# Performance work log

Hardware: AMD Instinct MI355X
Metric: run time of the kernel (lower is better)

The kernel has to match this reference:

```python
import jax, jax.numpy as jnp
import numpy as np

SCORE_THRESHOLD = 0.5
IOU_THRESHOLD = 0.5


def _pairwise_iou(boxes):
    # boxes: [N, 4] in xyxy
    x1, y1, x2, y2 = boxes[:, 0], boxes[:, 1], boxes[:, 2], boxes[:, 3]
    area = (x2 - x1) * (y2 - y1)  # [N]
    ix1 = jnp.maximum(x1[:, None], x1[None, :])
    iy1 = jnp.maximum(y1[:, None], y1[None, :])
    ix2 = jnp.minimum(x2[:, None], x2[None, :])
    iy2 = jnp.minimum(y2[:, None], y2[None, :])
    iw = jnp.clip(ix2 - ix1, 0.0)
    ih = jnp.clip(iy2 - iy1, 0.0)
    inter = iw * ih  # [N, N]
    union = area[:, None] + area[None, :] - inter
    return inter / jnp.maximum(union, 1e-9)


def setup_inputs() -> dict:
    key = jax.random.key(0)
    rtdetr_raw_out = jax.random.uniform(key, (1, 8192, 5), dtype=jnp.float32)
    return {"rtdetr_raw_out": rtdetr_raw_out}


def reference(rtdetr_raw_out):
    x = rtdetr_raw_out[0]                      # [N, 5]
    cxcywh = x[:, :4]
    conf = x[:, 4]
    conf = conf / jnp.max(conf)                # normalize by max score
    cx, cy, w, h = cxcywh[:, 0], cxcywh[:, 1], cxcywh[:, 2], cxcywh[:, 3]
    xyxy = jnp.stack([cx - w * 0.5, cy - h * 0.5, cx + w * 0.5, cy + h * 0.5], axis=1)
    valid = conf >= SCORE_THRESHOLD            # score filter
    N = xyxy.shape[0]
    # sort by descending score (torchvision nms processes boxes in score order)
    order = jnp.argsort(-conf)
    boxes_s = xyxy[order]
    scores_s = conf[order]
    valid_s = valid[order]
    iou = _pairwise_iou(boxes_s)               # [N, N]
    idx = jnp.arange(N)

    def body(i, keep):
        # if box i survives, suppress all lower-score boxes with IoU > thr
        sup = keep[i] & (iou[i] > IOU_THRESHOLD) & (idx > i)
        return keep & ~sup

    keep = jax.lax.fori_loop(0, N, body, valid_s)
    out = jnp.concatenate([boxes_s, scores_s[:, None]], axis=1)  # [N, 5]
    # fixed-shape output: suppressed / below-threshold rows are zeroed
    return jnp.where(keep[:, None], out, 0.0)
```

## Files before the change

### kernel.cpp

```cpp
#include <hip/hip_runtime.h>
#include <cstdint>

typedef unsigned long long ull;

#define N_BOX 8192
#define N_WORDS 128
#define CH 512
#define WPC 8
#define NBLK 16

#define OFF_TB     0
#define OFF_TC     3440640
#define OFF_TD     3932160
#define OFF_BOXES  4456448
#define OFF_SCORES 4587520
#define OFF_RANK   4620288
#define OFF_MAXC   4653056
#define OFF_CTRL   4653120
#define OFF_KEPT   4653248

__device__ __forceinline__ int rows_before2(int c) {
    return 7424 * c - 256 * c * c;
}

__device__ __forceinline__ ull make_key(float s, int idx) {
    return (((ull)__float_as_uint(s)) << 13) | (ull)(8191 - idx);
}

__device__ __forceinline__ float box_area(float4 b) {
    return __fmul_rn(__fsub_rn(b.z, b.x), __fsub_rn(b.w, b.y));
}

__device__ __forceinline__ bool iou_gt_half(float4 a, float aarea, float4 b, float barea) {
    float ix1 = fmaxf(a.x, b.x);
    float iy1 = fmaxf(a.y, b.y);
    float ix2 = fminf(a.z, b.z);
    float iy2 = fminf(a.w, b.w);
    float iw = fmaxf(__fsub_rn(ix2, ix1), 0.0f);
    float ih = fmaxf(__fsub_rn(iy2, iy1), 0.0f);
    float inter = __fmul_rn(iw, ih);
    float uni = __fsub_rn(__fadd_rn(aarea, barea), inter);
    float iou = __fdiv_rn(inter, fmaxf(uni, 1e-9f));
    return iou > 0.5f;
}

__global__ __launch_bounds__(256) void k1_max_zero(const float* __restrict__ in,
                                                   int* __restrict__ maxci,
                                                   int* __restrict__ rank,
                                                   int* __restrict__ ctrl) {
    int t = threadIdx.x;
    int i = blockIdx.x * 256 + t;
    float c = in[i * 5 + 4];
    for (int off = 32; off; off >>= 1) c = fmaxf(c, __shfl_down(c, off));
    __shared__ float wm[4];
    if ((t & 63) == 0) wm[t >> 6] = c;
    __syncthreads();
    if (t == 0) {
        float m = fmaxf(fmaxf(wm[0], wm[1]), fmaxf(wm[2], wm[3]));
        atomicMax(maxci, __float_as_int(m));
    }
    if (blockIdx.x == 0 && t < 32) ctrl[t] = 0;
    rank[i] = 0;
}

__global__ __launch_bounds__(256) void k2_rank(const float* __restrict__ in,
                                               const float* __restrict__ maxc_p,
                                               int* __restrict__ rank) {
    __shared__ ull keys[1024];
    int t = threadIdx.x;
    int bx = blockIdx.x;
    int it = bx & 31;
    int jt = bx >> 5;
    float maxc = *maxc_p;
    for (int r = 0; r < 4; ++r) {
        int j = jt * 1024 + r * 256 + t;
        float s = __fdiv_rn(in[j * 5 + 4], maxc);
        keys[r * 256 + t] = make_key(s, j);
    }
    __syncthreads();
    int i = it * 256 + t;
    ull ki = make_key(__fdiv_rn(in[i * 5 + 4], maxc), i);
    int cnt = 0;
    #pragma unroll 8
    for (int k = 0; k < 1024; ++k) cnt += (keys[k] > ki) ? 1 : 0;
    atomicAdd(&rank[i], cnt);
}

__global__ __launch_bounds__(256) void k3_scatter(const float* __restrict__ in,
                                                  const int* __restrict__ rank,
                                                  const float* __restrict__ maxc_p,
                                                  float4* __restrict__ boxes4,
                                                  float* __restrict__ scores,
                                                  int* __restrict__ ctrl) {
    int i = blockIdx.x * 256 + threadIdx.x;
    float cx = in[i * 5 + 0];
    float cy = in[i * 5 + 1];
    float w  = in[i * 5 + 2];
    float h  = in[i * 5 + 3];
    float c  = in[i * 5 + 4];
    float maxc = *maxc_p;
    float s = __fdiv_rn(c, maxc);
    int r = rank[i];
    float4 b;
    b.x = __fsub_rn(cx, __fmul_rn(w, 0.5f));
    b.y = __fsub_rn(cy, __fmul_rn(h, 0.5f));
    b.z = __fadd_rn(cx, __fmul_rn(w, 0.5f));
    b.w = __fadd_rn(cy, __fmul_rn(h, 0.5f));
    boxes4[r] = b;
    scores[r] = s;
    ull bal = __ballot(s >= 0.5f);
    if ((threadIdx.x & 63) == 0) atomicAdd(&ctrl[16], (int)__popcll(bal));
}

__global__ __launch_bounds__(256) void k4_build(const float4* __restrict__ boxes4,
                                                const float* __restrict__ scores,
                                                ull* __restrict__ TB,
                                                ull* __restrict__ TC,
                                                ull* __restrict__ TD) {
    __shared__ float4 sb[CH];
    __shared__ float sa[CH];
    int bid = blockIdx.x;
    int t = threadIdx.x;
    int c;
    int mode;
    int j0;
    if (bid >= 1920) {
        mode = 2;
        int d = bid - 1920;
        c = d >> 4;
        j0 = (d & 15) * 32;
    } else if (bid >= 1680) {
        mode = 1;
        int d = bid - 1680;
        c = d >> 4;
        j0 = (d & 15) * 32;
    } else {
        mode = 0;
        c = 0;
        int rem = bid;
        while (rem >= 224 - 16 * c) { rem -= 224 - 16 * c; ++c; }
        j0 = CH * (c + 2) + rem * 32;
    }
    if (scores[c * CH] < 0.5f) return;
    if (mode == 0 && scores[j0] < 0.5f) return;

    for (int i = t; i < CH; i += 256) {
        float4 b = boxes4[c * CH + i];
        sb[i] = b;
        sa[i] = box_area(b);
    }
    __syncthreads();

    int w = t & 7;
    int r = t >> 3;
    if (mode == 2) {
        int jl = j0 + r;
        float4 me = sb[jl];
        float ma = sa[jl];
        int wj = jl >> 6;
        int lim = (w < wj) ? 64 : ((w == wj) ? (jl & 63) : 0);
        ull bits = 0;
        for (int k = 0; k < lim; ++k)
            if (iou_gt_half(sb[w * 64 + k], sa[w * 64 + k], me, ma)) bits |= 1ull << k;
        TD[c * 4096 + w * 512 + jl] = bits;
    } else if (mode == 1) {
        int jl = j0 + r;
        int j = CH * (c + 1) + jl;
        float4 me = boxes4[j];
        float ma = box_area(me);
        ull bits = 0;
        for (int k = 0; k < 64; ++k)
            if (iou_gt_half(sb[w * 64 + k], sa[w * 64 + k], me, ma)) bits |= 1ull << k;
        TC[c * 4096 + w * 512 + jl] = bits;
    } else {
        int j = j0 + r;
        float4 me = boxes4[j];
        float ma = box_area(me);
        ull bits = 0;
        for (int k = 0; k < 64; ++k)
            if (iou_gt_half(sb[w * 64 + k], sa[w * 64 + k], me, ma)) bits |= 1ull << k;
        TB[(size_t)(rows_before2(c) + (j - CH * (c + 2))) * WPC + w] = bits;
    }
}

__global__ __launch_bounds__(1024) void k5_nms(const float4* __restrict__ boxes4,
                                               const float* __restrict__ scores,
                                               const ull* __restrict__ TBg,
                                               const ull* __restrict__ TCg,
                                               const ull* __restrict__ TDg,
                                               ull* __restrict__ keptg,
                                               int* __restrict__ ctrl,
                                               float* __restrict__ out) {
    __shared__ ull TDs[CH * WPC];
    __shared__ ull TCs[CH * WPC];
    __shared__ ull kwsh[WPC];
    __shared__ unsigned amask[16];
    int c = blockIdx.x;
    int t = threadIdx.x;
    int lane = t & 63;
    int wave = t >> 6;
    int vb = ctrl[16];
    int nchv = (vb + CH - 1) / CH;

    if (c < nchv) {
        {
            const ulonglong2* src = (const ulonglong2*)(TDg + (size_t)c * CH * WPC);
            ulonglong2* dst = (ulonglong2*)TDs;
            #pragma unroll
            for (int i2 = t; i2 < CH * WPC / 2; i2 += 1024) dst[i2] = src[i2];
        }
        if (c > 0) {
            const ulonglong2* src = (const ulonglong2*)(TCg + (size_t)(c - 1) * CH * WPC);
            ulonglong2* dst = (ulonglong2*)TCs;
            #pragma unroll
            for (int i2 = t; i2 < CH * WPC / 2; i2 += 1024) dst[i2] = src[i2];
        }
        if (t < 16) {
            int n = vb - (c * 16 + t) * 32;
            amask[t] = (n >= 32) ? 0xffffffffu : ((n <= 0) ? 0u : ((1u << n) - 1u));
        }
        __syncthreads();

        for (int cp = 0; cp + 2 <= c; ++cp) {
            if (wave == 0) {
                if (lane == 0) { while (atomicAdd(&ctrl[cp], 0) == 0) {} }
                __threadfence();
                if (lane < WPC)
                    kwsh[lane] = atomicAdd(&keptg[cp * WPC + lane], 0ull);
            }
            __syncthreads();
            ull anyk = kwsh[0] | kwsh[1] | kwsh[2] | kwsh[3] |
                       kwsh[4] | kwsh[5] | kwsh[6] | kwsh[7];
            if (anyk && t < CH) {
                if ((amask[t >> 5] >> (t & 31)) & 1u) {
                    const ull* row = TBg +
                        (size_t)(rows_before2(cp) + (c * CH + t - CH * (cp + 2))) * WPC;
                    ull a = 0;
                    #pragma unroll
                    for (int q = 0; q < WPC; ++q) a |= row[q] & kwsh[q];
                    if (a) atomicAnd(&amask[t >> 5], ~(1u << (t & 31)));
                }
            }
            __syncthreads();
        }

        if (c > 0) {
            if (wave == 0) {
                if (lane == 0) { while (atomicAdd(&ctrl[c - 1], 0) == 0) {} }
                __threadfence();
                if (lane < WPC)
                    kwsh[lane] = atomicAdd(&keptg[(c - 1) * WPC + lane], 0ull);
            }
            __syncthreads();
            if (wave < WPC) {
                bool dead = false;
                #pragma unroll
                for (int w = 0; w < WPC; ++w) {
                    ull kw = kwsh[w];
                    if (kw) dead |= (TCs[w * 512 + wave * 64 + lane] & kw) != 0ull;
                }
                ull d = __ballot(dead);
                if (lane == 0 && d) {
                    amask[2 * wave]     &= ~(unsigned)d;
                    amask[2 * wave + 1] &= ~(unsigned)(d >> 32);
                }
            }
            __syncthreads();
        }

        if (wave == 0) {
            ull alive[WPC];
            #pragma unroll
            for (int w = 0; w < WPC; ++w)
                alive[w] = (ull)amask[2 * w] | ((ull)amask[2 * w + 1] << 32);
            const ull* T = TDs;
            #pragma unroll
            for (int w = 0; w < WPC; ++w) {
                ull word = alive[w];
                if (!word) continue;
                ull Tc[WPC];
                #pragma unroll
                for (int j = 0; j < WPC; ++j)
                    if (j >= w) Tc[j] = T[w * 512 + j * 64 + lane];
                ull td = Tc[w];
                ull a2 = word, kept = 0;
                while (a2 & ~kept) {
                    bool al = (a2 >> lane) & 1;
                    bool kp = (kept >> lane) & 1;
                    ull nk = __ballot(al && !kp && ((td & a2) == 0));
                    ull nd = __ballot(al && !kp && ((td & kept) != 0));
                    kept |= nk;
                    a2 &= ~nd;
                }
                alive[w] = kept;
                #pragma unroll
                for (int j = 0; j < WPC; ++j) {
                    if (j <= w) continue;
                    if (!alive[j]) continue;
                    alive[j] &= ~__ballot((Tc[j] & kept) != 0);
                }
            }
            if (lane == 0) {
                #pragma unroll
                for (int w = 0; w < WPC; ++w) {
                    atomicExch(&keptg[c * WPC + w], alive[w]);
                    amask[2 * w]     = (unsigned)alive[w];
                    amask[2 * w + 1] = (unsigned)(alive[w] >> 32);
                }
            }
            __threadfence();
            if (lane == 0) atomicExch(&ctrl[c], 1);
        }
        __syncthreads();
    } else {
        if (t < 16) amask[t] = 0u;
        __syncthreads();
    }

    if (t < CH) {
        int j = c * CH + t;
        bool kept = (amask[t >> 5] >> (t & 31)) & 1u;
        float4 b = boxes4[j];
        float s = scores[j];
        out[j * 5 + 0] = kept ? b.x : 0.0f;
        out[j * 5 + 1] = kept ? b.y : 0.0f;
        out[j * 5 + 2] = kept ? b.z : 0.0f;
        out[j * 5 + 3] = kept ? b.w : 0.0f;
        out[j * 5 + 4] = kept ? s   : 0.0f;
    }
}

extern "C" void kernel_launch(void* const* d_in, const int* in_sizes, int n_in,
                              void* d_out, int out_size, void* d_ws, size_t ws_size,
                              hipStream_t stream) {
    const float* in = (const float*)d_in[0];
    char* ws = (char*)d_ws;
    ull* TB        = (ull*)(ws + OFF_TB);
    ull* TC        = (ull*)(ws + OFF_TC);
    ull* TD        = (ull*)(ws + OFF_TD);
    float4* boxes4 = (float4*)(ws + OFF_BOXES);
    float* scores  = (float*)(ws + OFF_SCORES);
    int* rank      = (int*)(ws + OFF_RANK);
    float* maxc    = (float*)(ws + OFF_MAXC);
    int* ctrl      = (int*)(ws + OFF_CTRL);
    ull* keptg     = (ull*)(ws + OFF_KEPT);
    float* out     = (float*)d_out;

    k1_max_zero<<<32, 256, 0, stream>>>(in, (int*)maxc, rank, ctrl);
    k2_rank<<<256, 256, 0, stream>>>(in, maxc, rank);
    k3_scatter<<<32, 256, 0, stream>>>(in, rank, maxc, boxes4, scores, ctrl);
    k4_build<<<2176, 256, 0, stream>>>(boxes4, scores, TB, TC, TD);
    k5_nms<<<NBLK, 1024, 0, stream>>>(boxes4, scores, TB, TC, TD, keptg, ctrl, out);
}
```

Measured before the change: 124.9 us.

## Fuse max, rank and scatter into one kernel; use acquire/release flags

Three preprocessing kernels (max reduction, pairwise rank counting, scatter) are merged into a single kernel. Each block redundantly loads all scores into shared memory, computes the max itself, and ranks 32 boxes using 8 threads per box with shuffle reductions. This removes two launches and the global rank/max atomics. The NMS inter-block signalling drops atomicAdd polling and threadfences in favour of acquire/release atomic loads and stores, with ctrl and kept words padded to separate cache lines. The cost is redundant per-block score loading and max computation.

```diff
diff --git a/kernel.cpp b/kernel.cpp
--- a/kernel.cpp
+++ b/kernel.cpp
@@ -14,17 +14,14 @@
 #define OFF_TD     3932160
 #define OFF_BOXES  4456448
 #define OFF_SCORES 4587520
-#define OFF_RANK   4620288
-#define OFF_MAXC   4653056
-#define OFF_CTRL   4653120
-#define OFF_KEPT   4653248
+#define OFF_CTRL   4620288
+#define OFF_KEPT   4624384
+
+#define CTRL_VB   512
+#define KSTRIDE   16
 
 __device__ __forceinline__ int rows_before2(int c) {
     return 7424 * c - 256 * c * c;
-}
-
-__device__ __forceinline__ ull make_key(float s, int idx) {
-    return (((ull)__float_as_uint(s)) << 13) | (ull)(8191 - idx);
 }
 
 __device__ __forceinline__ float box_area(float4 b) {
@@ -44,72 +41,67 @@
     return iou > 0.5f;
 }
 
-__global__ __launch_bounds__(256) void k1_max_zero(const float* __restrict__ in,
-                                                   int* __restrict__ maxci,
-                                                   int* __restrict__ rank,
-                                                   int* __restrict__ ctrl) {
-    int t = threadIdx.x;
-    int i = blockIdx.x * 256 + t;
-    float c = in[i * 5 + 4];
-    for (int off = 32; off; off >>= 1) c = fmaxf(c, __shfl_down(c, off));
+__global__ __launch_bounds__(256) void kA_rank_scatter(const float* __restrict__ in,
+                                                       float4* __restrict__ boxes4,
+                                                       float* __restrict__ scores,
+                                                       int* __restrict__ ctrl) {
+    __shared__ float sc[N_BOX];
     __shared__ float wm[4];
-    if ((t & 63) == 0) wm[t >> 6] = c;
-    __syncthreads();
-    if (t == 0) {
-        float m = fmaxf(fmaxf(wm[0], wm[1]), fmaxf(wm[2], wm[3]));
-        atomicMax(maxci, __float_as_int(m));
-    }
-    if (blockIdx.x == 0 && t < 32) ctrl[t] = 0;
-    rank[i] = 0;
-}
-
-__global__ __launch_bounds__(256) void k2_rank(const float* __restrict__ in,
-                                               const float* __restrict__ maxc_p,
-                                               int* __restrict__ rank) {
-    __shared__ ull keys[1024];
+    __shared__ int wv[4];
     int t = threadIdx.x;
     int bx = blockIdx.x;
-    int it = bx & 31;
-    int jt = bx >> 5;
-    float maxc = *maxc_p;
-    for (int r = 0; r < 4; ++r) {
-        int j = jt * 1024 + r * 256 + t;
-        float s = __fdiv_rn(in[j * 5 + 4], maxc);
-        keys[r * 256 + t] = make_key(s, j);
-    }
+
+    for (int k = t; k < N_BOX; k += 256) sc[k] = in[k * 5 + 4];
     __syncthreads();
-    int i = it * 256 + t;
-    ull ki = make_key(__fdiv_rn(in[i * 5 + 4], maxc), i);
+
+    float m = 0.0f;
+    for (int k = t; k < N_BOX; k += 256) m = fmaxf(m, sc[k]);
+    for (int off = 32; off; off >>= 1) m = fmaxf(m, __shfl_down(m, off));
+    if ((t & 63) == 0) wm[t >> 6] = m;
+    __syncthreads();
+    float maxc = fmaxf(fmaxf(wm[0], wm[1]), fmaxf(wm[2], wm[3]));
+
+    for (int k = t; k < N_BOX; k += 256) sc[k] = __fdiv_rn(sc[k], maxc);
+    __syncthreads();
+
+    int il = t >> 3, seg = t & 7;
+    int i = bx * 32 + il;
+    float si = sc[i];
+    int base = seg * 1024;
     int cnt = 0;
     #pragma unroll 8
-    for (int k = 0; k < 1024; ++k) cnt += (keys[k] > ki) ? 1 : 0;
-    atomicAdd(&rank[i], cnt);
-}
-
-__global__ __launch_bounds__(256) void k3_scatter(const float* __restrict__ in,
-                                                  const int* __restrict__ rank,
-                                                  const float* __restrict__ maxc_p,
-                                                  float4* __restrict__ boxes4,
-                                                  float* __restrict__ scores,
-                                                  int* __restrict__ ctrl) {
-    int i = blockIdx.x * 256 + threadIdx.x;
-    float cx = in[i * 5 + 0];
-    float cy = in[i * 5 + 1];
-    float w  = in[i * 5 + 2];
-    float h  = in[i * 5 + 3];
-    float c  = in[i * 5 + 4];
-    float maxc = *maxc_p;
-    float s = __fdiv_rn(c, maxc);
-    int r = rank[i];
-    float4 b;
-    b.x = __fsub_rn(cx, __fmul_rn(w, 0.5f));
-    b.y = __fsub_rn(cy, __fmul_rn(h, 0.5f));
-    b.z = __fadd_rn(cx, __fmul_rn(w, 0.5f));
-    b.w = __fadd_rn(cy, __fmul_rn(h, 0.5f));
-    boxes4[r] = b;
-    scores[r] = s;
-    ull bal = __ballot(s >= 0.5f);
-    if ((threadIdx.x & 63) == 0) atomicAdd(&ctrl[16], (int)__popcll(bal));
+    for (int cc = 0; cc < 1024; ++cc) {
+        int k = base + ((cc + seg) & 1023);
+        float sj = sc[k];
+        cnt += (sj > si || (sj == si && k < i)) ? 1 : 0;
+    }
+    cnt += __shfl_down(cnt, 4, 8);
+    cnt += __shfl_down(cnt, 2, 8);
+    cnt += __shfl_down(cnt, 1, 8);
+    if (seg == 0) {
+        int r = cnt;
+        float cx = in[i * 5 + 0];
+        float cy = in[i * 5 + 1];
+        float w  = in[i * 5 + 2];
+        float h  = in[i * 5 + 3];
+        float4 b;
+        b.x = __fsub_rn(cx, __fmul_rn(w, 0.5f));
+        b.y = __fsub_rn(cy, __fmul_rn(h, 0.5f));
+        b.z = __fadd_rn(cx, __fmul_rn(w, 0.5f));
+        b.w = __fadd_rn(cy, __fmul_rn(h, 0.5f));
+        boxes4[r] = b;
+        scores[r] = si;
+    }
+
+    if (bx == 0) {
+        int cv = 0;
+        for (int k = t; k < N_BOX; k += 256) cv += (sc[k] >= 0.5f) ? 1 : 0;
+        for (int off = 32; off; off >>= 1) cv += __shfl_down(cv, off);
+        if ((t & 63) == 0) wv[t >> 6] = cv;
+        if (t < NBLK) ctrl[t * 32] = 0;
+        __syncthreads();
+        if (t == 0) ctrl[CTRL_VB] = wv[0] + wv[1] + wv[2] + wv[3];
+    }
 }
 
 __global__ __launch_bounds__(256) void k4_build(const float4* __restrict__ boxes4,
@@ -199,7 +191,7 @@
     int t = threadIdx.x;
     int lane = t & 63;
     int wave = t >> 6;
-    int vb = ctrl[16];
+    int vb = ctrl[CTRL_VB];
     int nchv = (vb + CH - 1) / CH;
 
     if (c < nchv) {
@@ -222,11 +214,14 @@
         __syncthreads();
 
         for (int cp = 0; cp + 2 <= c; ++cp) {
-            if (wave == 0) {
-                if (lane == 0) { while (atomicAdd(&ctrl[cp], 0) == 0) {} }
-                __threadfence();
-                if (lane < WPC)
-                    kwsh[lane] = atomicAdd(&keptg[cp * WPC + lane], 0ull);
+            if (wave == 0 && lane == 0) {
+                while (__hip_atomic_load(&ctrl[cp * 32], __ATOMIC_ACQUIRE,
+                                         __HIP_MEMORY_SCOPE_AGENT) == 0) {}
+                #pragma unroll
+                for (int w = 0; w < WPC; ++w)
+                    kwsh[w] = __hip_atomic_load(&keptg[cp * KSTRIDE + w],
+                                                __ATOMIC_RELAXED,
+                                                __HIP_MEMORY_SCOPE_AGENT);
             }
             __syncthreads();
             ull anyk = kwsh[0] | kwsh[1] | kwsh[2] | kwsh[3] |
@@ -245,11 +240,14 @@
         }
 
         if (c > 0) {
-            if (wave == 0) {
-                if (lane == 0) { while (atomicAdd(&ctrl[c - 1], 0) == 0) {} }
-                __threadfence();
-                if (lane < WPC)
-                    kwsh[lane] = atomicAdd(&keptg[(c - 1) * WPC + lane], 0ull);
+            if (wave == 0 && lane == 0) {
+                while (__hip_atomic_load(&ctrl[(c - 1) * 32], __ATOMIC_ACQUIRE,
+                                         __HIP_MEMORY_SCOPE_AGENT) == 0) {}
+                #pragma unroll
+                for (int w = 0; w < WPC; ++w)
+                    kwsh[w] = __hip_atomic_load(&keptg[(c - 1) * KSTRIDE + w],
+                                                __ATOMIC_RELAXED,
+                                                __HIP_MEMORY_SCOPE_AGENT);
             }
             __syncthreads();
             if (wave < WPC) {
@@ -303,13 +301,14 @@
             if (lane == 0) {
                 #pragma unroll
                 for (int w = 0; w < WPC; ++w) {
-                    atomicExch(&keptg[c * WPC + w], alive[w]);
+                    __hip_atomic_store(&keptg[c * KSTRIDE + w], alive[w],
+                                       __ATOMIC_RELAXED, __HIP_MEMORY_SCOPE_AGENT);
                     amask[2 * w]     = (unsigned)alive[w];
                     amask[2 * w + 1] = (unsigned)(alive[w] >> 32);
                 }
-            }
-            __threadfence();
-            if (lane == 0) atomicExch(&ctrl[c], 1);
+                __hip_atomic_store(&ctrl[c * 32], 1,
+                                   __ATOMIC_RELEASE, __HIP_MEMORY_SCOPE_AGENT);
+            }
         }
         __syncthreads();
     } else {
@@ -340,15 +339,11 @@
     ull* TD        = (ull*)(ws + OFF_TD);
     float4* boxes4 = (float4*)(ws + OFF_BOXES);
     float* scores  = (float*)(ws + OFF_SCORES);
-    int* rank      = (int*)(ws + OFF_RANK);
-    float* maxc    = (float*)(ws + OFF_MAXC);
     int* ctrl      = (int*)(ws + OFF_CTRL);
     ull* keptg     = (ull*)(ws + OFF_KEPT);
     float* out     = (float*)d_out;
 
-    k1_max_zero<<<32, 256, 0, stream>>>(in, (int*)maxc, rank, ctrl);
-    k2_rank<<<256, 256, 0, stream>>>(in, maxc, rank);
-    k3_scatter<<<32, 256, 0, stream>>>(in, rank, maxc, boxes4, scores, ctrl);
+    kA_rank_scatter<<<256, 256, 0, stream>>>(in, boxes4, scores, ctrl);
     k4_build<<<2176, 256, 0, stream>>>(boxes4, scores, TB, TC, TD);
     k5_nms<<<NBLK, 1024, 0, stream>>>(boxes4, scores, TB, TC, TD, keptg, ctrl, out);
 }
```

Result: slower. 190.6 us (+52.5%).
